# Performance work log

Hardware: AMD Instinct MI355X
Metric: run time of the kernel (lower is better)

Reference implementation:

```python
import jax, jax.numpy as jnp
import numpy as np

B, T, D = 64, 2048, 256


def setup_inputs() -> dict:
    key = jax.random.key(0)
    k_x, k_len, k_w, k_b, k_a = jax.random.split(key, 5)
    xs = jax.random.normal(k_x, (B, T, D), dtype=jnp.float32)
    # ragged lengths -> prefix mask, mimicking per-sample slicing in the torch loop
    lens = jax.random.randint(k_len, (B,), T // 4, T + 1)
    mask = (jnp.arange(T)[None, :] < lens[:, None]).astype(jnp.int32)
    mask2 = jnp.ones((B, T), dtype=jnp.int32)  # unused by the module
    W = jax.random.normal(k_w, (D, D), dtype=jnp.float32) * (1.0 / np.sqrt(D))
    b = jax.random.normal(k_b, (D,), dtype=jnp.float32) * 0.01
    attn = jax.random.normal(k_a, (D,), dtype=jnp.float32)  # nn.Parameter(D,1) squeezed
    return {"xs": xs, "mask": mask, "mask2": mask2, "W": W, "b": b, "attn": attn}


def reference(xs, mask, mask2, W, b, attn):
    # h = tanh(Linear(x)); torch Linear: x @ W.T + b
    h = jnp.tanh(jnp.einsum("btd,ed->bte", xs, W) + b)          # [B,T,D]
    scores = jnp.einsum("btd,d->bt", h, attn)                    # [B,T]
    valid = mask.astype(bool)
    scores = jnp.where(valid, scores, -jnp.inf)                  # softmax over valid frames only
    w = jax.nn.softmax(scores, axis=1)[..., None]                # [B,T,1]
    mu = jnp.sum(xs * w, axis=1)                                 # [B,D]
    var = jnp.maximum(jnp.sum(xs * xs * w, axis=1) - mu * mu, 1e-5)
    return jnp.concatenate([mu, jnp.sqrt(var)], axis=1)          # [B,2D]
```

## Files before the change

### kernel.cpp

```cpp
#include <hip/hip_runtime.h>
#include <hip/hip_bf16.h>
#include <math.h>

#define PB 64
#define PT 2048
#define PD 256
#define PM (PB * PT)
#define SBM 64
#define NTILES (PM / SBM)
#define TPB (PT / SBM)

typedef __bf16 bf16x8 __attribute__((ext_vector_type(8)));
typedef short  s16x8  __attribute__((ext_vector_type(8)));
typedef float  f32x4  __attribute__((ext_vector_type(4)));

__device__ __forceinline__ short rne_bf16(float x) {
    unsigned u = __builtin_bit_cast(unsigned, x);
    return (short)((u + 0x7fffu + ((u >> 16) & 1u)) >> 16);
}

__device__ __forceinline__ void split_bf16(float x, short& hi, short& lo) {
    unsigned u = __builtin_bit_cast(unsigned, x);
    hi = (short)(u >> 16);
    float hf = __builtin_bit_cast(float, u & 0xffff0000u);
    lo = rne_bf16(x - hf);
}

__global__ __launch_bounds__(256) void prep_kernel(
    const float* __restrict__ W, short* __restrict__ Whi, short* __restrict__ Wlo)
{
    const int idx = blockIdx.x * 256 + threadIdx.x;
    const int e = idx >> 8;
    const int k = idx & 255;
    short h, l;
    split_bf16(W[idx], h, l);
    const int flat = (((e >> 4) * 8 + (k >> 5)) * 64 + ((k & 31) >> 3) * 16 + (e & 15)) * 8 + (k & 7);
    Whi[flat] = h;
    Wlo[flat] = l;
}

__global__ __launch_bounds__(512, 2) void score_kernel(
    const float* __restrict__ xs, const short* __restrict__ Whi,
    const short* __restrict__ Wlo, const float* __restrict__ bias,
    const float* __restrict__ attn, const int* __restrict__ mask,
    float* __restrict__ stats, float* __restrict__ part)
{
    __shared__ __align__(16) short Ah[4 * 8 * 64 * 8];
    __shared__ float sred[8][64];
    __shared__ float lw[64];

    const int tid  = threadIdx.x;
    const int lane = tid & 63;
    const int w    = tid >> 6;
    const int quad = lane >> 4;
    const int nl   = lane & 15;
    const int blk  = blockIdx.x;

    bf16x8 Bh[2][8], Bl[2][8];
#pragma unroll
    for (int n = 0; n < 2; ++n) {
#pragma unroll
        for (int kt = 0; kt < 8; ++kt) {
            const int nt   = w * 2 + n;
            const int bidx = ((nt * 8 + kt) * 64 + lane) * 8;
            Bh[n][kt] = *(const bf16x8*)&Whi[bidx];
            Bl[n][kt] = *(const bf16x8*)&Wlo[bidx];
        }
    }
    float bv[2], av[2];
#pragma unroll
    for (int n = 0; n < 2; ++n) {
        const int col = w * 32 + n * 16 + nl;
        bv[n] = bias[col];
        av[n] = attn[col];
    }

    for (int i = 0; i < 8; ++i) {
        const int tile = (blk & 63) * 32 + i * 4 + (blk >> 6);
        const int bm   = tile * SBM;

        const int mv = mask[bm + lane];
        if (__ballot(mv != 0) == 0ull) {
            if (tid == 0) { stats[tile * 2] = -INFINITY; stats[tile * 2 + 1] = 0.f; }
            continue;
        }

        __syncthreads();

#pragma unroll
        for (int p = 0; p < 4; ++p) {
            const int r  = p * 16 + (tid >> 5);
            const int kb = tid & 31;
            const float4 a0 = *(const float4*)&xs[(bm + r) * PD + kb * 8];
            const float4 a1 = *(const float4*)&xs[(bm + r) * PD + kb * 8 + 4];
            const float f[8] = {a0.x, a0.y, a0.z, a0.w, a1.x, a1.y, a1.z, a1.w};
            s16x8 h;
#pragma unroll
            for (int j = 0; j < 8; ++j) h[j] = rne_bf16(f[j]);
            const int mt = r >> 4, m_loc = r & 15;
            const int kt = kb >> 2, qd = kb & 3;
            const int msw = m_loc ^ (kb & 7);
            *(s16x8*)&Ah[(((mt * 8 + kt) * 64) + qd * 16 + msw) * 8] = h;
        }
        __syncthreads();

        f32x4 acc[4][2] = {};
#pragma unroll
        for (int kt = 0; kt < 8; ++kt) {
            s16x8 ah[4];
            const int msw = nl ^ ((kt * 4 + quad) & 7);
#pragma unroll
            for (int m = 0; m < 4; ++m)
                ah[m] = *(const s16x8*)&Ah[((m * 8 + kt) * 64 + quad * 16 + msw) * 8];
#pragma unroll
            for (int m = 0; m < 4; ++m) {
                const bf16x8 ahm = __builtin_bit_cast(bf16x8, ah[m]);
#pragma unroll
                for (int n = 0; n < 2; ++n) {
                    acc[m][n] = __builtin_amdgcn_mfma_f32_16x16x32_bf16(ahm, Bh[n][kt], acc[m][n], 0, 0, 0);
                    acc[m][n] = __builtin_amdgcn_mfma_f32_16x16x32_bf16(ahm, Bl[n][kt], acc[m][n], 0, 0, 0);
                }
            }
        }

#pragma unroll
        for (int m = 0; m < 4; ++m) {
            float rs[4] = {0.f, 0.f, 0.f, 0.f};
#pragma unroll
            for (int n = 0; n < 2; ++n) {
#pragma unroll
                for (int r = 0; r < 4; ++r) {
                    const float u  = acc[m][n][r] + bv[n];
                    const float e2 = __expf(2.f * u);
                    const float th = 1.f - 2.f * __builtin_amdgcn_rcpf(e2 + 1.f);
                    rs[r] = fmaf(th, av[n], rs[r]);
                }
            }
#pragma unroll
            for (int off = 1; off < 16; off <<= 1) {
#pragma unroll
                for (int r = 0; r < 4; ++r) rs[r] += __shfl_xor(rs[r], off);
            }
            if (nl == 0) {
#pragma unroll
                for (int r = 0; r < 4; ++r) sred[w][m * 16 + quad * 4 + r] = rs[r];
            }
        }
        __syncthreads();

        if (tid < 64) {
            float s = sred[0][tid] + sred[1][tid] + sred[2][tid] + sred[3][tid]
                    + sred[4][tid] + sred[5][tid] + sred[6][tid] + sred[7][tid];
            const bool vld = (mv != 0);
            s = vld ? s : -INFINITY;
            float mx = s;
#pragma unroll
            for (int off = 1; off < 64; off <<= 1) mx = fmaxf(mx, __shfl_xor(mx, off));
            const float wt = vld ? __expf(s - mx) : 0.f;
            float zs = wt;
#pragma unroll
            for (int off = 1; off < 64; off <<= 1) zs += __shfl_xor(zs, off);
            lw[tid] = wt;
            if (tid == 0) { stats[tile * 2] = mx; stats[tile * 2 + 1] = zs; }
        }
        __syncthreads();

        float4* rmu = (float4*)Ah;
        float4* rm2 = rmu + 8 * 64;
        float4 mu = {0.f, 0.f, 0.f, 0.f};
        float4 m2 = {0.f, 0.f, 0.f, 0.f};
#pragma unroll
        for (int j = 0; j < 8; ++j) {
            const int r  = w * 8 + j;
            const float wv = lw[r];
            const float4 x = *(const float4*)&xs[(bm + r) * PD + lane * 4];
            mu.x = fmaf(wv, x.x, mu.x); mu.y = fmaf(wv, x.y, mu.y);
            mu.z = fmaf(wv, x.z, mu.z); mu.w = fmaf(wv, x.w, mu.w);
            m2.x = fmaf(wv * x.x, x.x, m2.x); m2.y = fmaf(wv * x.y, x.y, m2.y);
            m2.z = fmaf(wv * x.z, x.z, m2.z); m2.w = fmaf(wv * x.w, x.w, m2.w);
        }
        rmu[w * 64 + lane] = mu;
        rm2[w * 64 + lane] = m2;
        __syncthreads();

        if (tid < 64) {
            float4 smu = rmu[tid], sm2 = rm2[tid];
#pragma unroll
            for (int q = 1; q < 8; ++q) {
                const float4 a = rmu[q * 64 + tid], d = rm2[q * 64 + tid];
                smu.x += a.x; smu.y += a.y; smu.z += a.z; smu.w += a.w;
                sm2.x += d.x; sm2.y += d.y; sm2.z += d.z; sm2.w += d.w;
            }
            const int base = tile * 512;
            *(float4*)&part[base + tid * 4]       = smu;
            *(float4*)&part[base + 256 + tid * 4] = sm2;
        }
    }
}

__global__ __launch_bounds__(256) void finalize_kernel(
    const float* __restrict__ stats, const float* __restrict__ part,
    float* __restrict__ out)
{
    const int b = blockIdx.x;
    const int d = threadIdx.x;

    float M = -INFINITY;
#pragma unroll
    for (int t = 0; t < TPB; ++t) M = fmaxf(M, stats[(b * TPB + t) * 2]);

    float Z = 0.f, m1 = 0.f, m2 = 0.f;
#pragma unroll 4
    for (int t = 0; t < TPB; ++t) {
        const int g = b * TPB + t;
        const float zt = stats[g * 2 + 1];
        if (zt > 0.f) {
            const float f = __expf(stats[g * 2] - M);
            Z  = fmaf(zt, f, Z);
            m1 = fmaf(part[g * 512 + d],       f, m1);
            m2 = fmaf(part[g * 512 + 256 + d], f, m2);
        }
    }
    const float inv = 1.f / Z;
    m1 *= inv;
    m2 *= inv;
    const float var = fmaxf(m2 - m1 * m1, 1e-5f);
    out[b * 512 + d]       = m1;
    out[b * 512 + 256 + d] = sqrtf(var);
}

extern "C" void kernel_launch(void* const* d_in, const int* in_sizes, int n_in,
                              void* d_out, int out_size, void* d_ws, size_t ws_size,
                              hipStream_t stream) {
    const float* xs   = (const float*)d_in[0];
    const int*   mask = (const int*)d_in[1];
    const float* W    = (const float*)d_in[3];
    const float* bias = (const float*)d_in[4];
    const float* attn = (const float*)d_in[5];
    float* out = (float*)d_out;

    float* stats = (float*)d_ws;
    float* part  = stats + NTILES * 2;
    short* Whi   = (short*)(part + NTILES * 512);
    short* Wlo   = Whi + PD * PD;

    prep_kernel<<<PD * PD / 256, 256, 0, stream>>>(W, Whi, Wlo);
    score_kernel<<<256, 512, 0, stream>>>(xs, Whi, Wlo, bias, attn, mask, stats, part);
    finalize_kernel<<<PB, 256, 0, stream>>>(stats, part, out);
}
```

Before: 242.0 us.

## Launch one block per 128-row tile and stream W from cache per k-step

Replaces the persistent 256-block loop over 64-row tiles with one block per 128-row tile (1024 blocks), so the work is spread across many more workgroups and fully masked tiles exit right away. The W hi/lo fragments are no longer held in registers for the whole kernel; they are reloaded from global/L2 on each k-step. This frees registers and allows launch bounds of 4 blocks per CU. In exchange, every block re-reads W, and the accumulators for 8 m-tiles raise register pressure.

```diff
diff --git a/kernel.cpp b/kernel.cpp
--- a/kernel.cpp
+++ b/kernel.cpp
@@ -6,7 +6,7 @@
 #define PT 2048
 #define PD 256
 #define PM (PB * PT)
-#define SBM 64
+#define SBM 128
 #define NTILES (PM / SBM)
 #define TPB (PT / SBM)
 
@@ -39,34 +39,89 @@
     Wlo[flat] = l;
 }
 
-__global__ __launch_bounds__(512, 2) void score_kernel(
+__global__ __launch_bounds__(512, 4) void score_kernel(
     const float* __restrict__ xs, const short* __restrict__ Whi,
     const short* __restrict__ Wlo, const float* __restrict__ bias,
     const float* __restrict__ attn, const int* __restrict__ mask,
     float* __restrict__ stats, float* __restrict__ part)
 {
-    __shared__ __align__(16) short Ah[4 * 8 * 64 * 8];
-    __shared__ float sred[8][64];
-    __shared__ float lw[64];
+    __shared__ __align__(16) short Ah[8 * 8 * 64 * 8];
+    __shared__ float sred[8][128];
+    __shared__ float lw[128];
+    __shared__ int vflag[8];
 
     const int tid  = threadIdx.x;
     const int lane = tid & 63;
     const int w    = tid >> 6;
     const int quad = lane >> 4;
     const int nl   = lane & 15;
-    const int blk  = blockIdx.x;
-
-    bf16x8 Bh[2][8], Bl[2][8];
-#pragma unroll
-    for (int n = 0; n < 2; ++n) {
-#pragma unroll
-        for (int kt = 0; kt < 8; ++kt) {
+
+    const int blk   = blockIdx.x;
+    const int tile  = (blk & 63) * TPB + (blk >> 6);
+    const int bm    = tile * SBM;
+
+    const int mv = mask[bm + (tid & 127)];
+    {
+        const unsigned long long bal = __ballot(mv != 0);
+        if (lane == 0) vflag[w] = (bal != 0ull) ? 1 : 0;
+    }
+    __syncthreads();
+    const int any = vflag[0] | vflag[1] | vflag[2] | vflag[3]
+                  | vflag[4] | vflag[5] | vflag[6] | vflag[7];
+    if (!any) {
+        if (tid == 0) { stats[tile * 2] = -INFINITY; stats[tile * 2 + 1] = 0.f; }
+        return;
+    }
+
+#pragma unroll
+    for (int p = 0; p < 8; ++p) {
+        const int r  = p * 16 + (tid >> 5);
+        const int kb = tid & 31;
+        const float4 a0 = *(const float4*)&xs[(bm + r) * PD + kb * 8];
+        const float4 a1 = *(const float4*)&xs[(bm + r) * PD + kb * 8 + 4];
+        const float f[8] = {a0.x, a0.y, a0.z, a0.w, a1.x, a1.y, a1.z, a1.w};
+        s16x8 h;
+#pragma unroll
+        for (int j = 0; j < 8; ++j) h[j] = rne_bf16(f[j]);
+        const int mt = r >> 4, m_loc = r & 15;
+        const int kt = kb >> 2, qd = kb & 3;
+        const int msw = m_loc ^ (kb & 7);
+        *(s16x8*)&Ah[(((mt * 8 + kt) * 64) + qd * 16 + msw) * 8] = h;
+    }
+    __syncthreads();
+
+    f32x4 acc[8][2] = {};
+#pragma unroll 2
+    for (int kt = 0; kt < 8; ++kt) {
+        bf16x8 bh[2], bl[2];
+#pragma unroll
+        for (int n = 0; n < 2; ++n) {
             const int nt   = w * 2 + n;
             const int bidx = ((nt * 8 + kt) * 64 + lane) * 8;
-            Bh[n][kt] = *(const bf16x8*)&Whi[bidx];
-            Bl[n][kt] = *(const bf16x8*)&Wlo[bidx];
-        }
-    }
+            bh[n] = *(const bf16x8*)&Whi[bidx];
+            bl[n] = *(const bf16x8*)&Wlo[bidx];
+        }
+        const int msw = nl ^ ((kt * 4 + quad) & 7);
+#pragma unroll
+        for (int g = 0; g < 2; ++g) {
+            s16x8 ah[4];
+#pragma unroll
+            for (int mm = 0; mm < 4; ++mm) {
+                const int m = g * 4 + mm;
+                ah[mm] = *(const s16x8*)&Ah[((m * 8 + kt) * 64 + quad * 16 + msw) * 8];
+            }
+#pragma unroll
+            for (int mm = 0; mm < 4; ++mm) {
+                const bf16x8 ahm = __builtin_bit_cast(bf16x8, ah[mm]);
+#pragma unroll
+                for (int n = 0; n < 2; ++n) {
+                    acc[g * 4 + mm][n] = __builtin_amdgcn_mfma_f32_16x16x32_bf16(ahm, bh[n], acc[g * 4 + mm][n], 0, 0, 0);
+                    acc[g * 4 + mm][n] = __builtin_amdgcn_mfma_f32_16x16x32_bf16(ahm, bl[n], acc[g * 4 + mm][n], 0, 0, 0);
+                }
+            }
+        }
+    }
+
     float bv[2], av[2];
 #pragma unroll
     for (int n = 0; n < 2; ++n) {
@@ -74,127 +129,82 @@
         bv[n] = bias[col];
         av[n] = attn[col];
     }
-
-    for (int i = 0; i < 8; ++i) {
-        const int tile = (blk & 63) * 32 + i * 4 + (blk >> 6);
-        const int bm   = tile * SBM;
-
-        const int mv = mask[bm + lane];
-        if (__ballot(mv != 0) == 0ull) {
-            if (tid == 0) { stats[tile * 2] = -INFINITY; stats[tile * 2 + 1] = 0.f; }
-            continue;
-        }
-
-        __syncthreads();
-
-#pragma unroll
-        for (int p = 0; p < 4; ++p) {
-            const int r  = p * 16 + (tid >> 5);
-            const int kb = tid & 31;
-            const float4 a0 = *(const float4*)&xs[(bm + r) * PD + kb * 8];
-            const float4 a1 = *(const float4*)&xs[(bm + r) * PD + kb * 8 + 4];
-            const float f[8] = {a0.x, a0.y, a0.z, a0.w, a1.x, a1.y, a1.z, a1.w};
-            s16x8 h;
-#pragma unroll
-            for (int j = 0; j < 8; ++j) h[j] = rne_bf16(f[j]);
-            const int mt = r >> 4, m_loc = r & 15;
-            const int kt = kb >> 2, qd = kb & 3;
-            const int msw = m_loc ^ (kb & 7);
-            *(s16x8*)&Ah[(((mt * 8 + kt) * 64) + qd * 16 + msw) * 8] = h;
-        }
-        __syncthreads();
-
-        f32x4 acc[4][2] = {};
-#pragma unroll
-        for (int kt = 0; kt < 8; ++kt) {
-            s16x8 ah[4];
-            const int msw = nl ^ ((kt * 4 + quad) & 7);
-#pragma unroll
-            for (int m = 0; m < 4; ++m)
-                ah[m] = *(const s16x8*)&Ah[((m * 8 + kt) * 64 + quad * 16 + msw) * 8];
-#pragma unroll
-            for (int m = 0; m < 4; ++m) {
-                const bf16x8 ahm = __builtin_bit_cast(bf16x8, ah[m]);
-#pragma unroll
-                for (int n = 0; n < 2; ++n) {
-                    acc[m][n] = __builtin_amdgcn_mfma_f32_16x16x32_bf16(ahm, Bh[n][kt], acc[m][n], 0, 0, 0);
-                    acc[m][n] = __builtin_amdgcn_mfma_f32_16x16x32_bf16(ahm, Bl[n][kt], acc[m][n], 0, 0, 0);
-                }
+#pragma unroll
+    for (int m = 0; m < 8; ++m) {
+        float rs[4] = {0.f, 0.f, 0.f, 0.f};
+#pragma unroll
+        for (int n = 0; n < 2; ++n) {
+#pragma unroll
+            for (int r = 0; r < 4; ++r) {
+                const float u  = acc[m][n][r] + bv[n];
+                const float e2 = __expf(2.f * u);
+                const float th = 1.f - 2.f * __builtin_amdgcn_rcpf(e2 + 1.f);
+                rs[r] = fmaf(th, av[n], rs[r]);
             }
         }
-
-#pragma unroll
-        for (int m = 0; m < 4; ++m) {
-            float rs[4] = {0.f, 0.f, 0.f, 0.f};
-#pragma unroll
-            for (int n = 0; n < 2; ++n) {
-#pragma unroll
-                for (int r = 0; r < 4; ++r) {
-                    const float u  = acc[m][n][r] + bv[n];
-                    const float e2 = __expf(2.f * u);
-                    const float th = 1.f - 2.f * __builtin_amdgcn_rcpf(e2 + 1.f);
-                    rs[r] = fmaf(th, av[n], rs[r]);
-                }
-            }
-#pragma unroll
-            for (int off = 1; off < 16; off <<= 1) {
-#pragma unroll
-                for (int r = 0; r < 4; ++r) rs[r] += __shfl_xor(rs[r], off);
-            }
-            if (nl == 0) {
-#pragma unroll
-                for (int r = 0; r < 4; ++r) sred[w][m * 16 + quad * 4 + r] = rs[r];
-            }
-        }
-        __syncthreads();
-
-        if (tid < 64) {
-            float s = sred[0][tid] + sred[1][tid] + sred[2][tid] + sred[3][tid]
-                    + sred[4][tid] + sred[5][tid] + sred[6][tid] + sred[7][tid];
-            const bool vld = (mv != 0);
-            s = vld ? s : -INFINITY;
-            float mx = s;
-#pragma unroll
-            for (int off = 1; off < 64; off <<= 1) mx = fmaxf(mx, __shfl_xor(mx, off));
-            const float wt = vld ? __expf(s - mx) : 0.f;
-            float zs = wt;
-#pragma unroll
-            for (int off = 1; off < 64; off <<= 1) zs += __shfl_xor(zs, off);
-            lw[tid] = wt;
-            if (tid == 0) { stats[tile * 2] = mx; stats[tile * 2 + 1] = zs; }
-        }
-        __syncthreads();
-
-        float4* rmu = (float4*)Ah;
-        float4* rm2 = rmu + 8 * 64;
-        float4 mu = {0.f, 0.f, 0.f, 0.f};
-        float4 m2 = {0.f, 0.f, 0.f, 0.f};
-#pragma unroll
-        for (int j = 0; j < 8; ++j) {
-            const int r  = w * 8 + j;
-            const float wv = lw[r];
-            const float4 x = *(const float4*)&xs[(bm + r) * PD + lane * 4];
-            mu.x = fmaf(wv, x.x, mu.x); mu.y = fmaf(wv, x.y, mu.y);
-            mu.z = fmaf(wv, x.z, mu.z); mu.w = fmaf(wv, x.w, mu.w);
-            m2.x = fmaf(wv * x.x, x.x, m2.x); m2.y = fmaf(wv * x.y, x.y, m2.y);
-            m2.z = fmaf(wv * x.z, x.z, m2.z); m2.w = fmaf(wv * x.w, x.w, m2.w);
-        }
-        rmu[w * 64 + lane] = mu;
-        rm2[w * 64 + lane] = m2;
-        __syncthreads();
-
-        if (tid < 64) {
-            float4 smu = rmu[tid], sm2 = rm2[tid];
-#pragma unroll
-            for (int q = 1; q < 8; ++q) {
-                const float4 a = rmu[q * 64 + tid], d = rm2[q * 64 + tid];
-                smu.x += a.x; smu.y += a.y; smu.z += a.z; smu.w += a.w;
-                sm2.x += d.x; sm2.y += d.y; sm2.z += d.z; sm2.w += d.w;
-            }
-            const int base = tile * 512;
-            *(float4*)&part[base + tid * 4]       = smu;
-            *(float4*)&part[base + 256 + tid * 4] = sm2;
-        }
+#pragma unroll
+        for (int off = 1; off < 16; off <<= 1) {
+#pragma unroll
+            for (int r = 0; r < 4; ++r) rs[r] += __shfl_xor(rs[r], off);
+        }
+        if (nl == 0) {
+#pragma unroll
+            for (int r = 0; r < 4; ++r) sred[w][m * 16 + quad * 4 + r] = rs[r];
+        }
+    }
+    __syncthreads();
+
+    if (tid < 64) {
+        float s0 = 0.f, s1 = 0.f;
+#pragma unroll
+        for (int q = 0; q < 8; ++q) { s0 += sred[q][tid]; s1 += sred[q][tid + 64]; }
+        const bool v0 = (mask[bm + tid] != 0);
+        const bool v1 = (mask[bm + tid + 64] != 0);
+        s0 = v0 ? s0 : -INFINITY;
+        s1 = v1 ? s1 : -INFINITY;
+        float mx = fmaxf(s0, s1);
+#pragma unroll
+        for (int off = 1; off < 64; off <<= 1) mx = fmaxf(mx, __shfl_xor(mx, off));
+        const float w0 = v0 ? __expf(s0 - mx) : 0.f;
+        const float w1 = v1 ? __expf(s1 - mx) : 0.f;
+        float zs = w0 + w1;
+#pragma unroll
+        for (int off = 1; off < 64; off <<= 1) zs += __shfl_xor(zs, off);
+        lw[tid]      = w0;
+        lw[tid + 64] = w1;
+        if (tid == 0) { stats[tile * 2] = mx; stats[tile * 2 + 1] = zs; }
+    }
+    __syncthreads();
+
+    float4* rmu = (float4*)Ah;
+    float4* rm2 = rmu + 8 * 64;
+    float4 mu = {0.f, 0.f, 0.f, 0.f};
+    float4 m2 = {0.f, 0.f, 0.f, 0.f};
+#pragma unroll
+    for (int j = 0; j < 16; ++j) {
+        const int r  = w * 16 + j;
+        const float wv = lw[r];
+        const float4 x = *(const float4*)&xs[(bm + r) * PD + lane * 4];
+        mu.x = fmaf(wv, x.x, mu.x); mu.y = fmaf(wv, x.y, mu.y);
+        mu.z = fmaf(wv, x.z, mu.z); mu.w = fmaf(wv, x.w, mu.w);
+        m2.x = fmaf(wv * x.x, x.x, m2.x); m2.y = fmaf(wv * x.y, x.y, m2.y);
+        m2.z = fmaf(wv * x.z, x.z, m2.z); m2.w = fmaf(wv * x.w, x.w, m2.w);
+    }
+    rmu[w * 64 + lane] = mu;
+    rm2[w * 64 + lane] = m2;
+    __syncthreads();
+
+    if (tid < 64) {
+        float4 smu = rmu[tid], sm2 = rm2[tid];
+#pragma unroll
+        for (int q = 1; q < 8; ++q) {
+            const float4 a = rmu[q * 64 + tid], d = rm2[q * 64 + tid];
+            smu.x += a.x; smu.y += a.y; smu.z += a.z; smu.w += a.w;
+            sm2.x += d.x; sm2.y += d.y; sm2.z += d.z; sm2.w += d.w;
+        }
+        const int base = tile * 512;
+        *(float4*)&part[base + tid * 4]       = smu;
+        *(float4*)&part[base + 256 + tid * 4] = sm2;
     }
 }
 
@@ -245,6 +255,6 @@
     short* Wlo   = Whi + PD * PD;
 
     prep_kernel<<<PD * PD / 256, 256, 0, stream>>>(W, Whi, Wlo);
-    score_kernel<<<256, 512, 0, stream>>>(xs, Whi, Wlo, bias, attn, mask, stats, part);
+    score_kernel<<<NTILES, 512, 0, stream>>>(xs, Whi, Wlo, bias, attn, mask, stats, part);
     finalize_kernel<<<PB, 256, 0, stream>>>(stats, part, out);
 }
```

New measurement: 230.9 us. -4.6%, faster.
